# Kernel tuning notes

Measured on AMD Instinct MI355X. Metric: run time of the kernel, lower is better.

Reference implementation:

```python
import jax, jax.numpy as jnp
import numpy as np

N_NODES = 100_000
N_EDGES = 1_600_000
D_IN, D_H, D_OUT = 128, 128, 64


def setup_inputs() -> dict:
    key = jax.random.key(0)
    ks = jax.random.split(key, 8)
    x = jax.random.normal(ks[0], (N_NODES, D_IN), dtype=jnp.float32)
    edge_index = jax.random.randint(ks[1], (2, N_EDGES), 0, N_NODES, dtype=jnp.int32)
    def glorot(k, shape):
        lim = float(np.sqrt(6.0 / (shape[0] + shape[1])))
        return jax.random.uniform(k, shape, jnp.float32, -lim, lim)
    return {
        "x": x,
        "edge_index": edge_index,
        "W1": glorot(ks[2], (D_IN, D_H)),  "b1": jnp.zeros((D_H,), jnp.float32),
        "W2": glorot(ks[3], (D_H, D_H)),   "b2": jnp.zeros((D_H,), jnp.float32),
        "W3": glorot(ks[4], (D_H, D_OUT)), "b3": jnp.zeros((D_OUT,), jnp.float32),
    }


def gcn_conv(x, edge_index, W, b, num_nodes):
    # PyG GCNConv: add self-loops, symmetric D^-1/2 (A+I) D^-1/2 normalization,
    # linear transform before aggregation, then bias.
    xw = x @ W                                   # [N, D_out]
    loops = jnp.arange(num_nodes, dtype=edge_index.dtype)
    row = jnp.concatenate([edge_index[0], loops])  # source nodes
    col = jnp.concatenate([edge_index[1], loops])  # target nodes
    deg = jax.ops.segment_sum(jnp.ones_like(col, xw.dtype), col,
                              num_segments=num_nodes)
    dinv = jnp.where(deg > 0, jax.lax.rsqrt(jnp.maximum(deg, 1e-12)), 0.0)
    norm = dinv[row] * dinv[col]                 # [E+N]
    msg = xw[row] * norm[:, None]                # gather + scale
    out = jax.ops.segment_sum(msg, col, num_segments=num_nodes)
    return out + b


def reference(x, edge_index, W1, b1, W2, b2, W3, b3):
    # Dropout(0.2) is identity in eval/inference mode.
    h = jax.nn.relu(gcn_conv(x, edge_index, W1, b1, N_NODES))
    h = jax.nn.relu(gcn_conv(h, edge_index, W2, b2, N_NODES))
    return gcn_conv(h, edge_index, W3, b3, N_NODES)
```

## Files before the change

### kernel.cpp

```cpp
#include <hip/hip_runtime.h>

#define NN 100000
#define NE 1600000
constexpr int KDIM = 128;
constexpr int NPB = 128;
constexpr int G = (NN + NPB - 1) / NPB;
constexpr int CH = 8192;
constexpr int NCH = (NE + CH - 1) / CH;

typedef _Float16 f16x4 __attribute__((ext_vector_type(4)));
typedef _Float16 f16x8 __attribute__((ext_vector_type(8)));
typedef float f32x4 __attribute__((ext_vector_type(4)));
using half8 = f16x8;

__device__ __forceinline__ int swz(int byte) {
  return byte ^ (((byte >> 8) & 7) << 4);
}


__global__ __launch_bounds__(256) void k_zero(int* p, int n) {
  int i = blockIdx.x * 256 + threadIdx.x;
  if (i < n) p[i] = 0;
}

__global__ __launch_bounds__(256) void k_bhist(const int* __restrict__ col,
                                               int* __restrict__ bcnt) {
  __shared__ int h[G];
  for (int i = threadIdx.x; i < G; i += 256) h[i] = 0;
  __syncthreads();
  const int base = blockIdx.x * CH;
  const int m = min(CH, NE - base);
  for (int i = threadIdx.x; i < m; i += 256) atomicAdd(&h[col[base + i] >> 7], 1);
  __syncthreads();
  for (int i = threadIdx.x; i < G; i += 256)
    if (h[i]) atomicAdd(&bcnt[i], h[i]);
}

__global__ void k_bscan(const int* __restrict__ bcnt, int* __restrict__ bbase,
                        int* __restrict__ cursor) {
  __shared__ int sd[256];
  const int t = threadIdx.x;
  int v[4];
  int s = 0;
#pragma unroll
  for (int j = 0; j < 4; ++j) {
    int idx = t * 4 + j;
    v[j] = (idx < G) ? bcnt[idx] : 0;
    s += v[j];
  }
  sd[t] = s;
  __syncthreads();
  for (int off = 1; off < 256; off <<= 1) {
    int x = (t >= off) ? sd[t - off] : 0;
    __syncthreads();
    sd[t] += x;
    __syncthreads();
  }
  int run = sd[t] - s;
#pragma unroll
  for (int j = 0; j < 4; ++j) {
    int idx = t * 4 + j;
    if (idx < G) {
      bbase[idx] = run;
      cursor[idx] = run;
    }
    run += v[j];
  }
  if (t == 255) bbase[G] = run;
}

__global__ __launch_bounds__(256) void k_bucket(const int* __restrict__ row,
                                                const int* __restrict__ col,
                                                int* __restrict__ cursor,
                                                unsigned long long* __restrict__ temp) {
  __shared__ int h[G];
  for (int i = threadIdx.x; i < G; i += 256) h[i] = 0;
  __syncthreads();
  const int base = blockIdx.x * CH;
  const int m = min(CH, NE - base);
  for (int i = threadIdx.x; i < m; i += 256) atomicAdd(&h[col[base + i] >> 7], 1);
  __syncthreads();
  for (int i = threadIdx.x; i < G; i += 256) {
    int c = h[i];
    if (c) h[i] = atomicAdd(&cursor[i], c);
  }
  __syncthreads();
  for (int i = threadIdx.x; i < m; i += 256) {
    int cc = col[base + i];
    int rr = row[base + i];
    int slot = atomicAdd(&h[cc >> 7], 1);
    temp[slot] = ((unsigned long long)(unsigned)cc << 32) | (unsigned)rr;
  }
}

__global__ __launch_bounds__(256) void k_group(const unsigned long long* __restrict__ temp,
                                               const int* __restrict__ bbase,
                                               int* __restrict__ rowptr,
                                               float* __restrict__ dinv,
                                               int* __restrict__ srcs) {
  __shared__ int fill[NPB];
  __shared__ int nbase[NPB];
  __shared__ int sc[NPB];
  const int g = blockIdx.x, t = threadIdx.x;
  const int lo = g * NPB;
  const int b0 = bbase[g], b1 = bbase[g + 1];
  if (t < NPB) fill[t] = 0;
  __syncthreads();
  for (int s = b0 + t; s < b1; s += 256) {
    int cc = (int)(temp[s] >> 32);
    atomicAdd(&fill[cc & (NPB - 1)], 1);
  }
  __syncthreads();
  int v = 0;
  if (t < NPB) {
    v = fill[t];
    sc[t] = v;
  }
  __syncthreads();
  for (int off = 1; off < NPB; off <<= 1) {
    int x = 0;
    if (t < NPB && t >= off) x = sc[t - off];
    __syncthreads();
    if (t < NPB) sc[t] += x;
    __syncthreads();
  }
  if (t < NPB) {
    int excl = sc[t] - v;
    nbase[t] = b0 + excl;
    int node = lo + t;
    if (node < NN) {
      rowptr[node] = b0 + excl;
      dinv[node] = rsqrtf((float)(v + 1));
    }
    fill[t] = 0;
  }
  if (g == G - 1 && t == 0) rowptr[NN] = NE;
  __syncthreads();
  for (int s = b0 + t; s < b1; s += 256) {
    unsigned long long p = temp[s];
    int cc = (int)(p >> 32);
    int rr = (int)(unsigned)(p & 0xffffffffull);
    int c = cc & (NPB - 1);
    int slot = atomicAdd(&fill[c], 1);
    srcs[nbase[c] + slot] = rr;
  }
}

__global__ __launch_bounds__(256) void k_wconv(const float* __restrict__ W,
                                               _Float16* __restrict__ Wt, int N) {
  int i = blockIdx.x * 256 + threadIdx.x;
  if (i < 128 * N) {
    int k = i / N, c = i % N;
    Wt[c * 128 + k] = (_Float16)W[i];
  }
}

template <int BN, bool F32IN>
__global__ __launch_bounds__(256, 2) void k_gemm_mfma(const void* __restrict__ Ain,
                                                      const _Float16* __restrict__ Wt_g,
                                                      const float* __restrict__ dinv,
                                                      _Float16* __restrict__ Y, int M) {
  constexpr int NB = BN / 16;
  __shared__ _Float16 Ah[128 * 128];
  __shared__ _Float16 Wt[BN * 128];
  const int t = threadIdx.x;
  const int rbase = blockIdx.x * 128;

  for (int c = t; c < BN * 16; c += 256) {
    f16x8 v = *(const f16x8*)((const char*)Wt_g + c * 16);
    *(f16x8*)((char*)Wt + swz(c * 16)) = v;
  }
  if constexpr (F32IN) {
    const float* A = (const float*)Ain;
    for (int c = t; c < 2048; c += 256) {
      int r = c >> 4, kc = c & 15;
      int row = rbase + r;
      f16x8 h = {};
      if (row < M) {
        float dv = dinv[row];
        const float* p = A + (size_t)row * 128 + kc * 8;
        float4 u0 = *(const float4*)p;
        float4 u1 = *(const float4*)(p + 4);
        h[0] = (_Float16)(u0.x * dv);
        h[1] = (_Float16)(u0.y * dv);
        h[2] = (_Float16)(u0.z * dv);
        h[3] = (_Float16)(u0.w * dv);
        h[4] = (_Float16)(u1.x * dv);
        h[5] = (_Float16)(u1.y * dv);
        h[6] = (_Float16)(u1.z * dv);
        h[7] = (_Float16)(u1.w * dv);
      }
      *(f16x8*)((char*)Ah + swz(c * 16)) = h;
    }
  } else {
    const _Float16* A = (const _Float16*)Ain;
    for (int c = t; c < 2048; c += 256) {
      int r = c >> 4;
      int row = rbase + r;
      f16x8 h = {};
      if (row < M) h = *(const f16x8*)(A + (size_t)row * 128 + (c & 15) * 8);
      *(f16x8*)((char*)Ah + swz(c * 16)) = h;
    }
  }
  __syncthreads();

  const int wave = t >> 6, lane = t & 63;
  const int l16 = lane & 15, lk = lane >> 4;

  f32x4 acc[2][NB];
#pragma unroll
  for (int m = 0; m < 2; ++m)
#pragma unroll
    for (int n = 0; n < NB; ++n) acc[m][n] = (f32x4){0.f, 0.f, 0.f, 0.f};

#pragma unroll
  for (int ks = 0; ks < 4; ++ks) {
    const int kbyte = ks * 64 + lk * 16;
    f16x8 afr[2];
#pragma unroll
    for (int m = 0; m < 2; ++m) {
      int row = wave * 32 + m * 16 + l16;
      afr[m] = *(const f16x8*)((const char*)Ah + swz(row * 256 + kbyte));
    }
#pragma unroll
    for (int n = 0; n < NB; ++n) {
      int wrow = n * 16 + l16;
      f16x8 wfr = *(const f16x8*)((const char*)Wt + swz(wrow * 256 + kbyte));
#pragma unroll
      for (int m = 0; m < 2; ++m)
        acc[m][n] = __builtin_amdgcn_mfma_f32_16x16x32_f16(wfr, afr[m], acc[m][n], 0, 0, 0);
    }
  }

#pragma unroll
  for (int m = 0; m < 2; ++m) {
    int row = rbase + wave * 32 + m * 16 + l16;
    if (row < M) {
      _Float16* yr = Y + (size_t)row * BN + lk * 4;
#pragma unroll
      for (int n = 0; n < NB; ++n) {
        f16x4 h = {(_Float16)acc[m][n][0], (_Float16)acc[m][n][1],
                   (_Float16)acc[m][n][2], (_Float16)acc[m][n][3]};
        *(f16x4*)(yr + n * 16) = h;
      }
    }
  }
}

__global__ __launch_bounds__(256) void k_agg128h(const _Float16* __restrict__ Y,
                                                 const int* __restrict__ rowptr,
                                                 const int* __restrict__ srcs,
                                                 const float* __restrict__ dinv,
                                                 const float* __restrict__ bias,
                                                 _Float16* __restrict__ Out, int n) {
  const int wave = threadIdx.x >> 6;
  const int lane = threadIdx.x & 63;
  const int node = blockIdx.x * 4 + wave;
  if (node >= n) return;
  const int part = lane >> 4;
  const int q = lane & 15;
  const int jb = rowptr[node];
  const int je = rowptr[node + 1];

  float acc[8];
#pragma unroll
  for (int j = 0; j < 8; ++j) acc[j] = 0.f;
  if (part == 0) {
    half8 s = *(const half8*)(Y + (size_t)node * 128 + q * 8);
#pragma unroll
    for (int j = 0; j < 8; ++j) acc[j] = (float)s[j];
  }

  for (int j0 = jb; j0 < je; j0 += 64) {
    const int m = min(64, je - j0);
    int idx = 0;
    if (lane < m) idx = srcs[j0 + lane];
    const int full = m & ~15;
    int eb = 0;
    for (; eb < full; eb += 16) {
      const int e0 = eb + part;
      int s0 = __shfl(idx, e0);
      int s1 = __shfl(idx, e0 + 4);
      int s2 = __shfl(idx, e0 + 8);
      int s3 = __shfl(idx, e0 + 12);
      half8 v0 = *(const half8*)(Y + (size_t)s0 * 128 + q * 8);
      half8 v1 = *(const half8*)(Y + (size_t)s1 * 128 + q * 8);
      half8 v2 = *(const half8*)(Y + (size_t)s2 * 128 + q * 8);
      half8 v3 = *(const half8*)(Y + (size_t)s3 * 128 + q * 8);
#pragma unroll
      for (int j = 0; j < 8; ++j)
        acc[j] += ((float)v0[j] + (float)v1[j]) + ((float)v2[j] + (float)v3[j]);
    }
    if (eb < m) {
      const int e0 = eb + part;
      int s0 = __shfl(idx, e0);
      int s1 = __shfl(idx, e0 + 4);
      int s2 = __shfl(idx, e0 + 8);
      int s3 = __shfl(idx, e0 + 12);
      half8 v0 = *(const half8*)(Y + (size_t)s0 * 128 + q * 8);
      half8 v1 = *(const half8*)(Y + (size_t)s1 * 128 + q * 8);
      half8 v2 = *(const half8*)(Y + (size_t)s2 * 128 + q * 8);
      half8 v3 = *(const half8*)(Y + (size_t)s3 * 128 + q * 8);
      const float m0 = (e0 < m) ? 1.f : 0.f;
      const float m1 = (e0 + 4 < m) ? 1.f : 0.f;
      const float m2 = (e0 + 8 < m) ? 1.f : 0.f;
      const float m3 = (e0 + 12 < m) ? 1.f : 0.f;
#pragma unroll
      for (int j = 0; j < 8; ++j)
        acc[j] += (m0 * (float)v0[j] + m1 * (float)v1[j]) +
                  (m2 * (float)v2[j] + m3 * (float)v3[j]);
    }
  }

#pragma unroll
  for (int j = 0; j < 8; ++j) {
    acc[j] += __shfl_xor(acc[j], 16);
    acc[j] += __shfl_xor(acc[j], 32);
  }

  if (part == 0) {
    const float dv = dinv[node];
    f16x8 h;
#pragma unroll
    for (int j = 0; j < 8; ++j) {
      float o = fmaf(acc[j], dv, bias[q * 8 + j]);
      o = fmaxf(o, 0.f);
      h[j] = (_Float16)(o * dv);
    }
    *(f16x8*)(Out + (size_t)node * 128 + q * 8) = h;
  }
}

__global__ __launch_bounds__(256) void k_agg64h(const _Float16* __restrict__ Y,
                                                const int* __restrict__ rowptr,
                                                const int* __restrict__ srcs,
                                                const float* __restrict__ dinv,
                                                const float* __restrict__ bias,
                                                float* __restrict__ Out, int n) {
  const int wave = threadIdx.x >> 6;
  const int lane = threadIdx.x & 63;
  const int node = blockIdx.x * 4 + wave;
  if (node >= n) return;
  const int part = lane >> 3;
  const int q = lane & 7;
  const int jb = rowptr[node];
  const int je = rowptr[node + 1];

  float acc[8];
#pragma unroll
  for (int j = 0; j < 8; ++j) acc[j] = 0.f;
  if (part == 0) {
    half8 s = *(const half8*)(Y + (size_t)node * 64 + q * 8);
#pragma unroll
    for (int j = 0; j < 8; ++j) acc[j] = (float)s[j];
  }

  for (int j0 = jb; j0 < je; j0 += 64) {
    const int m = min(64, je - j0);
    int idx = 0;
    if (lane < m) idx = srcs[j0 + lane];
    const int full = m & ~31;
    int eb = 0;
    for (; eb < full; eb += 32) {
      const int e0 = eb + part;
      int s0 = __shfl(idx, e0);
      int s1 = __shfl(idx, e0 + 8);
      int s2 = __shfl(idx, e0 + 16);
      int s3 = __shfl(idx, e0 + 24);
      half8 v0 = *(const half8*)(Y + (size_t)s0 * 64 + q * 8);
      half8 v1 = *(const half8*)(Y + (size_t)s1 * 64 + q * 8);
      half8 v2 = *(const half8*)(Y + (size_t)s2 * 64 + q * 8);
      half8 v3 = *(const half8*)(Y + (size_t)s3 * 64 + q * 8);
#pragma unroll
      for (int j = 0; j < 8; ++j)
        acc[j] += ((float)v0[j] + (float)v1[j]) + ((float)v2[j] + (float)v3[j]);
    }
    if (eb < m) {
      const int e0 = eb + part;
      int s0 = __shfl(idx, e0);
      int s1 = __shfl(idx, e0 + 8);
      int s2 = __shfl(idx, e0 + 16);
      int s3 = __shfl(idx, e0 + 24);
      half8 v0 = *(const half8*)(Y + (size_t)s0 * 64 + q * 8);
      half8 v1 = *(const half8*)(Y + (size_t)s1 * 64 + q * 8);
      half8 v2 = *(const half8*)(Y + (size_t)s2 * 64 + q * 8);
      half8 v3 = *(const half8*)(Y + (size_t)s3 * 64 + q * 8);
      const float m0 = (e0 < m) ? 1.f : 0.f;
      const float m1 = (e0 + 8 < m) ? 1.f : 0.f;
      const float m2 = (e0 + 16 < m) ? 1.f : 0.f;
      const float m3 = (e0 + 24 < m) ? 1.f : 0.f;
#pragma unroll
      for (int j = 0; j < 8; ++j)
        acc[j] += (m0 * (float)v0[j] + m1 * (float)v1[j]) +
                  (m2 * (float)v2[j] + m3 * (float)v3[j]);
    }
  }

#pragma unroll
  for (int j = 0; j < 8; ++j) {
    acc[j] += __shfl_xor(acc[j], 8);
    acc[j] += __shfl_xor(acc[j], 16);
    acc[j] += __shfl_xor(acc[j], 32);
  }

  if (part == 0) {
    const float dv = dinv[node];
    float o[8];
#pragma unroll
    for (int j = 0; j < 8; ++j) o[j] = fmaf(acc[j], dv, bias[q * 8 + j]);
    float* orow = Out + (size_t)node * 64 + q * 8;
    *(float4*)(orow) = make_float4(o[0], o[1], o[2], o[3]);
    *(float4*)(orow + 4) = make_float4(o[4], o[5], o[6], o[7]);
  }
}


extern "C" void kernel_launch(void* const* d_in, const int* in_sizes, int n_in,
                              void* d_out, int out_size, void* d_ws, size_t ws_size,
                              hipStream_t stream) {
  const float* x = (const float*)d_in[0];
  const int* ei = (const int*)d_in[1];
  const float* W1 = (const float*)d_in[2];
  const float* b1 = (const float*)d_in[3];
  const float* W2 = (const float*)d_in[4];
  const float* b2 = (const float*)d_in[5];
  const float* W3 = (const float*)d_in[6];
  const float* b3 = (const float*)d_in[7];
  float* out = (float*)d_out;

  const int* erow = ei;
  const int* ecol = ei + NE;

  char* w = (char*)d_ws;
  auto alloc = [&](size_t b) {
    char* p = w;
    w += (b + 255) & ~(size_t)255;
    return (void*)p;
  };
  float* dinv = (float*)alloc((size_t)NN * 4);
  int* rowptr = (int*)alloc((size_t)(NN + 1) * 4);
  int* bcnt = (int*)alloc((size_t)(G + 1) * 4);
  int* bbase = (int*)alloc((size_t)(G + 1) * 4);
  int* cursor = (int*)alloc((size_t)G * 4);
  int* srcs = (int*)alloc((size_t)NE * 4);
  _Float16* w1h = (_Float16*)alloc((size_t)128 * 128 * 2);
  _Float16* w2h = (_Float16*)alloc((size_t)128 * 128 * 2);
  _Float16* w3h = (_Float16*)alloc((size_t)128 * 64 * 2);
  _Float16* ybuf = (_Float16*)alloc((size_t)NN * 128 * 2);
  _Float16* hbuf = (_Float16*)alloc((size_t)NN * 128 * 2);
  unsigned long long* temp = (unsigned long long*)ybuf;

  k_zero<<<(G + 255) / 256, 256, 0, stream>>>(bcnt, G);
  k_bhist<<<NCH, 256, 0, stream>>>(ecol, bcnt);
  k_bscan<<<1, 256, 0, stream>>>(bcnt, bbase, cursor);
  k_bucket<<<NCH, 256, 0, stream>>>(erow, ecol, cursor, temp);
  k_group<<<G, 256, 0, stream>>>(temp, bbase, rowptr, dinv, srcs);

  k_wconv<<<64, 256, 0, stream>>>(W1, w1h, 128);
  k_wconv<<<64, 256, 0, stream>>>(W2, w2h, 128);
  k_wconv<<<32, 256, 0, stream>>>(W3, w3h, 64);

  const int nbG = (NN + 127) / 128;
  const int nbA = (NN + 3) / 4;

  k_gemm_mfma<128, true><<<nbG, 256, 0, stream>>>(x, w1h, dinv, ybuf, NN);
  k_agg128h<<<nbA, 256, 0, stream>>>(ybuf, rowptr, srcs, dinv, b1, hbuf, NN);
  k_gemm_mfma<128, false><<<nbG, 256, 0, stream>>>(hbuf, w2h, dinv, ybuf, NN);
  k_agg128h<<<nbA, 256, 0, stream>>>(ybuf, rowptr, srcs, dinv, b2, hbuf, NN);
  k_gemm_mfma<64, false><<<nbG, 256, 0, stream>>>(hbuf, w3h, dinv, ybuf, NN);
  k_agg64h<<<nbA, 256, 0, stream>>>(ybuf, rowptr, srcs, dinv, b3, out, NN);
}
```

Before: 284.6 us.

## Use fixed-capacity bucket slots, fuse weight conversion, pad aggregation with zero row

After: 267.9 us. 1.06x faster.

```diff
diff --git a/kernel.cpp b/kernel.cpp
--- a/kernel.cpp
+++ b/kernel.cpp
@@ -7,6 +7,7 @@
 constexpr int G = (NN + NPB - 1) / NPB;
 constexpr int CH = 8192;
 constexpr int NCH = (NE + CH - 1) / CH;
+constexpr int CAP = 4000;
 
 typedef _Float16 f16x4 __attribute__((ext_vector_type(4)));
 typedef _Float16 f16x8 __attribute__((ext_vector_type(8)));
@@ -23,8 +24,10 @@
   if (i < n) p[i] = 0;
 }
 
-__global__ __launch_bounds__(256) void k_bhist(const int* __restrict__ col,
-                                               int* __restrict__ bcnt) {
+__global__ __launch_bounds__(256) void k_bucketP(const int* __restrict__ row,
+                                                 const int* __restrict__ col,
+                                                 int* __restrict__ cursor,
+                                                 unsigned long long* __restrict__ temp) {
   __shared__ int h[G];
   for (int i = threadIdx.x; i < G; i += 256) h[i] = 0;
   __syncthreads();
@@ -32,12 +35,21 @@
   const int m = min(CH, NE - base);
   for (int i = threadIdx.x; i < m; i += 256) atomicAdd(&h[col[base + i] >> 7], 1);
   __syncthreads();
-  for (int i = threadIdx.x; i < G; i += 256)
-    if (h[i]) atomicAdd(&bcnt[i], h[i]);
-}
-
-__global__ void k_bscan(const int* __restrict__ bcnt, int* __restrict__ bbase,
-                        int* __restrict__ cursor) {
+  for (int i = threadIdx.x; i < G; i += 256) {
+    int c = h[i];
+    if (c) h[i] = atomicAdd(&cursor[i], c);
+  }
+  __syncthreads();
+  for (int i = threadIdx.x; i < m; i += 256) {
+    int cc = col[base + i];
+    int rr = row[base + i];
+    int slot = atomicAdd(&h[cc >> 7], 1);
+    temp[(size_t)(cc >> 7) * CAP + slot] =
+        ((unsigned long long)(unsigned)cc << 32) | (unsigned)rr;
+  }
+}
+
+__global__ void k_bscan(const int* __restrict__ cnt, int* __restrict__ bbase) {
   __shared__ int sd[256];
   const int t = threadIdx.x;
   int v[4];
@@ -45,7 +57,7 @@
 #pragma unroll
   for (int j = 0; j < 4; ++j) {
     int idx = t * 4 + j;
-    v[j] = (idx < G) ? bcnt[idx] : 0;
+    v[j] = (idx < G) ? cnt[idx] : 0;
     s += v[j];
   }
   sd[t] = s;
@@ -60,54 +72,29 @@
 #pragma unroll
   for (int j = 0; j < 4; ++j) {
     int idx = t * 4 + j;
-    if (idx < G) {
-      bbase[idx] = run;
-      cursor[idx] = run;
-    }
+    if (idx < G) bbase[idx] = run;
     run += v[j];
   }
   if (t == 255) bbase[G] = run;
 }
 
-__global__ __launch_bounds__(256) void k_bucket(const int* __restrict__ row,
-                                                const int* __restrict__ col,
-                                                int* __restrict__ cursor,
-                                                unsigned long long* __restrict__ temp) {
-  __shared__ int h[G];
-  for (int i = threadIdx.x; i < G; i += 256) h[i] = 0;
-  __syncthreads();
-  const int base = blockIdx.x * CH;
-  const int m = min(CH, NE - base);
-  for (int i = threadIdx.x; i < m; i += 256) atomicAdd(&h[col[base + i] >> 7], 1);
-  __syncthreads();
-  for (int i = threadIdx.x; i < G; i += 256) {
-    int c = h[i];
-    if (c) h[i] = atomicAdd(&cursor[i], c);
-  }
-  __syncthreads();
-  for (int i = threadIdx.x; i < m; i += 256) {
-    int cc = col[base + i];
-    int rr = row[base + i];
-    int slot = atomicAdd(&h[cc >> 7], 1);
-    temp[slot] = ((unsigned long long)(unsigned)cc << 32) | (unsigned)rr;
-  }
-}
-
-__global__ __launch_bounds__(256) void k_group(const unsigned long long* __restrict__ temp,
-                                               const int* __restrict__ bbase,
-                                               int* __restrict__ rowptr,
-                                               float* __restrict__ dinv,
-                                               int* __restrict__ srcs) {
+__global__ __launch_bounds__(256) void k_groupP(const unsigned long long* __restrict__ temp,
+                                                const int* __restrict__ bbase,
+                                                int* __restrict__ rowptr,
+                                                float* __restrict__ dinv,
+                                                int* __restrict__ srcs) {
   __shared__ int fill[NPB];
   __shared__ int nbase[NPB];
   __shared__ int sc[NPB];
   const int g = blockIdx.x, t = threadIdx.x;
   const int lo = g * NPB;
-  const int b0 = bbase[g], b1 = bbase[g + 1];
+  const int b0 = bbase[g];
+  const int n = bbase[g + 1] - b0;
+  const unsigned long long* tp = temp + (size_t)g * CAP;
   if (t < NPB) fill[t] = 0;
   __syncthreads();
-  for (int s = b0 + t; s < b1; s += 256) {
-    int cc = (int)(temp[s] >> 32);
+  for (int s = t; s < n; s += 256) {
+    int cc = (int)(tp[s] >> 32);
     atomicAdd(&fill[cc & (NPB - 1)], 1);
   }
   __syncthreads();
@@ -136,8 +123,8 @@
   }
   if (g == G - 1 && t == 0) rowptr[NN] = NE;
   __syncthreads();
-  for (int s = b0 + t; s < b1; s += 256) {
-    unsigned long long p = temp[s];
+  for (int s = t; s < n; s += 256) {
+    unsigned long long p = tp[s];
     int cc = (int)(p >> 32);
     int rr = (int)(unsigned)(p & 0xffffffffull);
     int c = cc & (NPB - 1);
@@ -146,12 +133,24 @@
   }
 }
 
-__global__ __launch_bounds__(256) void k_wconv(const float* __restrict__ W,
-                                               _Float16* __restrict__ Wt, int N) {
+__global__ __launch_bounds__(256) void k_wconvAll(const float* __restrict__ W1,
+                                                  const float* __restrict__ W2,
+                                                  const float* __restrict__ W3,
+                                                  _Float16* __restrict__ w1h,
+                                                  _Float16* __restrict__ w2h,
+                                                  _Float16* __restrict__ w3h) {
   int i = blockIdx.x * 256 + threadIdx.x;
-  if (i < 128 * N) {
-    int k = i / N, c = i % N;
-    Wt[c * 128 + k] = (_Float16)W[i];
+  if (i < 16384) {
+    int k = i >> 7, c = i & 127;
+    w1h[c * 128 + k] = (_Float16)W1[i];
+  } else if (i < 32768) {
+    int j = i - 16384;
+    int k = j >> 7, c = j & 127;
+    w2h[c * 128 + k] = (_Float16)W2[j];
+  } else if (i < 40960) {
+    int j = i - 32768;
+    int k = j >> 6, c = j & 63;
+    w3h[c * 128 + k] = (_Float16)W3[j];
   }
 }
 
@@ -209,40 +208,45 @@
 
   f32x4 acc[2][NB];
 #pragma unroll
-  for (int m = 0; m < 2; ++m)
-#pragma unroll
-    for (int n = 0; n < NB; ++n) acc[m][n] = (f32x4){0.f, 0.f, 0.f, 0.f};
+  for (int mm = 0; mm < 2; ++mm)
+#pragma unroll
+    for (int n = 0; n < NB; ++n) acc[mm][n] = (f32x4){0.f, 0.f, 0.f, 0.f};
 
 #pragma unroll
   for (int ks = 0; ks < 4; ++ks) {
     const int kbyte = ks * 64 + lk * 16;
     f16x8 afr[2];
 #pragma unroll
-    for (int m = 0; m < 2; ++m) {
-      int row = wave * 32 + m * 16 + l16;
-      afr[m] = *(const f16x8*)((const char*)Ah + swz(row * 256 + kbyte));
+    for (int mm = 0; mm < 2; ++mm) {
+      int row = wave * 32 + mm * 16 + l16;
+      afr[mm] = *(const f16x8*)((const char*)Ah + swz(row * 256 + kbyte));
     }
 #pragma unroll
     for (int n = 0; n < NB; ++n) {
       int wrow = n * 16 + l16;
       f16x8 wfr = *(const f16x8*)((const char*)Wt + swz(wrow * 256 + kbyte));
 #pragma unroll
-      for (int m = 0; m < 2; ++m)
-        acc[m][n] = __builtin_amdgcn_mfma_f32_16x16x32_f16(wfr, afr[m], acc[m][n], 0, 0, 0);
-    }
-  }
-
-#pragma unroll
-  for (int m = 0; m < 2; ++m) {
-    int row = rbase + wave * 32 + m * 16 + l16;
+      for (int mm = 0; mm < 2; ++mm)
+        acc[mm][n] = __builtin_amdgcn_mfma_f32_16x16x32_f16(wfr, afr[mm], acc[mm][n], 0, 0, 0);
+    }
+  }
+
+#pragma unroll
+  for (int mm = 0; mm < 2; ++mm) {
+    int row = rbase + wave * 32 + mm * 16 + l16;
     if (row < M) {
       _Float16* yr = Y + (size_t)row * BN + lk * 4;
 #pragma unroll
       for (int n = 0; n < NB; ++n) {
-        f16x4 h = {(_Float16)acc[m][n][0], (_Float16)acc[m][n][1],
-                   (_Float16)acc[m][n][2], (_Float16)acc[m][n][3]};
+        f16x4 h = {(_Float16)acc[mm][n][0], (_Float16)acc[mm][n][1],
+                   (_Float16)acc[mm][n][2], (_Float16)acc[mm][n][3]};
         *(f16x4*)(yr + n * 16) = h;
       }
+    } else if (row == M) {
+      _Float16* yr = Y + (size_t)row * BN + lk * 4;
+      f16x4 z = {};
+#pragma unroll
+      for (int n = 0; n < NB; ++n) *(f16x4*)(yr + n * 16) = z;
     }
   }
 }
@@ -273,11 +277,8 @@
 
   for (int j0 = jb; j0 < je; j0 += 64) {
     const int m = min(64, je - j0);
-    int idx = 0;
-    if (lane < m) idx = srcs[j0 + lane];
-    const int full = m & ~15;
-    int eb = 0;
-    for (; eb < full; eb += 16) {
+    const int idx = (lane < m) ? srcs[j0 + lane] : NN;
+    for (int eb = 0; eb < m; eb += 16) {
       const int e0 = eb + part;
       int s0 = __shfl(idx, e0);
       int s1 = __shfl(idx, e0 + 4);
@@ -287,28 +288,9 @@
       half8 v1 = *(const half8*)(Y + (size_t)s1 * 128 + q * 8);
       half8 v2 = *(const half8*)(Y + (size_t)s2 * 128 + q * 8);
       half8 v3 = *(const half8*)(Y + (size_t)s3 * 128 + q * 8);
-#pragma unroll
-      for (int j = 0; j < 8; ++j)
-        acc[j] += ((float)v0[j] + (float)v1[j]) + ((float)v2[j] + (float)v3[j]);
-    }
-    if (eb < m) {
-      const int e0 = eb + part;
-      int s0 = __shfl(idx, e0);
-      int s1 = __shfl(idx, e0 + 4);
-      int s2 = __shfl(idx, e0 + 8);
-      int s3 = __shfl(idx, e0 + 12);
-      half8 v0 = *(const half8*)(Y + (size_t)s0 * 128 + q * 8);
-      half8 v1 = *(const half8*)(Y + (size_t)s1 * 128 + q * 8);
-      half8 v2 = *(const half8*)(Y + (size_t)s2 * 128 + q * 8);
-      half8 v3 = *(const half8*)(Y + (size_t)s3 * 128 + q * 8);
-      const float m0 = (e0 < m) ? 1.f : 0.f;
-      const float m1 = (e0 + 4 < m) ? 1.f : 0.f;
-      const float m2 = (e0 + 8 < m) ? 1.f : 0.f;
-      const float m3 = (e0 + 12 < m) ? 1.f : 0.f;
-#pragma unroll
-      for (int j = 0; j < 8; ++j)
-        acc[j] += (m0 * (float)v0[j] + m1 * (float)v1[j]) +
-                  (m2 * (float)v2[j] + m3 * (float)v3[j]);
+      half8 s = (v0 + v1) + (v2 + v3);
+#pragma unroll
+      for (int j = 0; j < 8; ++j) acc[j] += (float)s[j];
     }
   }
 
@@ -357,11 +339,8 @@
 
   for (int j0 = jb; j0 < je; j0 += 64) {
     const int m = min(64, je - j0);
-    int idx = 0;
-    if (lane < m) idx = srcs[j0 + lane];
-    const int full = m & ~31;
-    int eb = 0;
-    for (; eb < full; eb += 32) {
+    const int idx = (lane < m) ? srcs[j0 + lane] : NN;
+    for (int eb = 0; eb < m; eb += 32) {
       const int e0 = eb + part;
       int s0 = __shfl(idx, e0);
       int s1 = __shfl(idx, e0 + 8);
@@ -371,28 +350,9 @@
       half8 v1 = *(const half8*)(Y + (size_t)s1 * 64 + q * 8);
       half8 v2 = *(const half8*)(Y + (size_t)s2 * 64 + q * 8);
       half8 v3 = *(const half8*)(Y + (size_t)s3 * 64 + q * 8);
-#pragma unroll
-      for (int j = 0; j < 8; ++j)
-        acc[j] += ((float)v0[j] + (float)v1[j]) + ((float)v2[j] + (float)v3[j]);
-    }
-    if (eb < m) {
-      const int e0 = eb + part;
-      int s0 = __shfl(idx, e0);
-      int s1 = __shfl(idx, e0 + 8);
-      int s2 = __shfl(idx, e0 + 16);
-      int s3 = __shfl(idx, e0 + 24);
-      half8 v0 = *(const half8*)(Y + (size_t)s0 * 64 + q * 8);
-      half8 v1 = *(const half8*)(Y + (size_t)s1 * 64 + q * 8);
-      half8 v2 = *(const half8*)(Y + (size_t)s2 * 64 + q * 8);
-      half8 v3 = *(const half8*)(Y + (size_t)s3 * 64 + q * 8);
-      const float m0 = (e0 < m) ? 1.f : 0.f;
-      const float m1 = (e0 + 8 < m) ? 1.f : 0.f;
-      const float m2 = (e0 + 16 < m) ? 1.f : 0.f;
-      const float m3 = (e0 + 24 < m) ? 1.f : 0.f;
-#pragma unroll
-      for (int j = 0; j < 8; ++j)
-        acc[j] += (m0 * (float)v0[j] + m1 * (float)v1[j]) +
-                  (m2 * (float)v2[j] + m3 * (float)v3[j]);
+      half8 s = (v0 + v1) + (v2 + v3);
+#pragma unroll
+      for (int j = 0; j < 8; ++j) acc[j] += (float)s[j];
     }
   }
 
@@ -439,26 +399,21 @@
   };
   float* dinv = (float*)alloc((size_t)NN * 4);
   int* rowptr = (int*)alloc((size_t)(NN + 1) * 4);
-  int* bcnt = (int*)alloc((size_t)(G + 1) * 4);
+  int* cursor = (int*)alloc((size_t)G * 4);
   int* bbase = (int*)alloc((size_t)(G + 1) * 4);
-  int* cursor = (int*)alloc((size_t)G * 4);
   int* srcs = (int*)alloc((size_t)NE * 4);
   _Float16* w1h = (_Float16*)alloc((size_t)128 * 128 * 2);
   _Float16* w2h = (_Float16*)alloc((size_t)128 * 128 * 2);
   _Float16* w3h = (_Float16*)alloc((size_t)128 * 64 * 2);
-  _Float16* ybuf = (_Float16*)alloc((size_t)NN * 128 * 2);
-  _Float16* hbuf = (_Float16*)alloc((size_t)NN * 128 * 2);
+  _Float16* ybuf = (_Float16*)alloc((size_t)(NN + 1) * 128 * 2);
+  _Float16* hbuf = (_Float16*)alloc((size_t)(NN + 1) * 128 * 2);
   unsigned long long* temp = (unsigned long long*)ybuf;
 
-  k_zero<<<(G + 255) / 256, 256, 0, stream>>>(bcnt, G);
-  k_bhist<<<NCH, 256, 0, stream>>>(ecol, bcnt);
-  k_bscan<<<1, 256, 0, stream>>>(bcnt, bbase, cursor);
-  k_bucket<<<NCH, 256, 0, stream>>>(erow, ecol, cursor, temp);
-  k_group<<<G, 256, 0, stream>>>(temp, bbase, rowptr, dinv, srcs);
-
-  k_wconv<<<64, 256, 0, stream>>>(W1, w1h, 128);
-  k_wconv<<<64, 256, 0, stream>>>(W2, w2h, 128);
-  k_wconv<<<32, 256, 0, stream>>>(W3, w3h, 64);
+  k_zero<<<(G + 255) / 256, 256, 0, stream>>>(cursor, G);
+  k_bucketP<<<NCH, 256, 0, stream>>>(erow, ecol, cursor, temp);
+  k_bscan<<<1, 256, 0, stream>>>(cursor, bbase);
+  k_groupP<<<G, 256, 0, stream>>>(temp, bbase, rowptr, dinv, srcs);
+  k_wconvAll<<<160, 256, 0, stream>>>(W1, W2, W3, w1h, w2h, w3h);
 
   const int nbG = (NN + 127) / 128;
   const int nbA = (NN + 3) / 4;
```
